# Kernel tuning notes

Hardware: AMD Instinct MI355X
Metric: run time of the kernel (lower is better)

## Reference

```python
import jax, jax.numpy as jnp
import numpy as np

B, T, H, IN, OUT, HORIZON = 65536, 15, 128, 6, 3, 10
LN_EPS = 1e-5


def _w(k, shape, s=0.08):
    return jax.random.normal(k, shape, jnp.float32) * s


def setup_inputs() -> dict:
    key = jax.random.key(0)
    ks = jax.random.split(key, 16)
    return {
        "x": jax.random.normal(ks[0], (B, T, IN), jnp.float32),
        # encoder layer 0 (input 6 -> 128), PyTorch LSTM gate order i,f,g,o
        "W_ih0": _w(ks[1], (4 * H, IN)), "W_hh0": _w(ks[2], (4 * H, H)), "b0": jnp.zeros((4 * H,), jnp.float32),
        # encoder layer 1 (128 -> 128)
        "W_ih1": _w(ks[3], (4 * H, H)), "W_hh1": _w(ks[4], (4 * H, H)), "b1": jnp.zeros((4 * H,), jnp.float32),
        # decoder LSTM (128 -> 128)
        "W_ihd": _w(ks[5], (4 * H, H)), "W_hhd": _w(ks[6], (4 * H, H)), "bd": jnp.zeros((4 * H,), jnp.float32),
        # step embedding [pred_horizon+1, H]
        "emb": _w(ks[7], (HORIZON + 1, H), 0.5),
        # decoder_input_proj: Linear(3+128 -> 128)
        "Wp": _w(ks[8], (H, OUT + H)), "bp": jnp.zeros((H,), jnp.float32),
        # heads
        "Wm": _w(ks[9], (OUT, H)), "bm": jnp.zeros((OUT,), jnp.float32),
        "Ws": _w(ks[10], (OUT, H)), "bs": jnp.zeros((OUT,), jnp.float32),
        # dec_ln
        "ln_g": jnp.ones((H,), jnp.float32), "ln_b": jnp.zeros((H,), jnp.float32),
    }


def _lstm_cell(h, c, x_t, Wih, Whh, b):
    g = x_t @ Wih.T + h @ Whh.T + b  # [B, 4H]
    i, f, gg, o = jnp.split(g, 4, axis=-1)
    c = jax.nn.sigmoid(f) * c + jax.nn.sigmoid(i) * jnp.tanh(gg)
    h = jax.nn.sigmoid(o) * jnp.tanh(c)
    return h, c


def _run_lstm_layer(seq, Wih, Whh, b):
    # seq: [B, T, D] -> outputs [B, T, H], final (h, c)
    n = seq.shape[0]
    h0 = jnp.zeros((n, H), seq.dtype)
    c0 = jnp.zeros((n, H), seq.dtype)

    def step(carry, xt):
        h, c = carry
        h, c = _lstm_cell(h, c, xt, Wih, Whh, b)
        return (h, c), h

    (h, c), outs = jax.lax.scan(step, (h0, c0), jnp.swapaxes(seq, 0, 1))
    return jnp.swapaxes(outs, 0, 1), h, c


def _layernorm(x, g, b):
    mu = jnp.mean(x, axis=-1, keepdims=True)
    var = jnp.mean(jnp.square(x - mu), axis=-1, keepdims=True)
    return (x - mu) * jax.lax.rsqrt(var + LN_EPS) * g + b


def reference(x, W_ih0, W_hh0, b0, W_ih1, W_hh1, b1, W_ihd, W_hhd, bd, emb, Wp, bp, Wm, bm, Ws, bs, ln_g, ln_b):
    # --- encoder: 2-layer LSTM (eval mode, no dropout) ---
    out0, _, _ = _run_lstm_layer(x, W_ih0, W_hh0, b0)
    _, h_enc, c_enc = _run_lstm_layer(out0, W_ih1, W_hh1, b1)

    prev0 = x[:, -1, :OUT]  # [B, 3]
    n = x.shape[0]

    def dstep(carry, step):
        h, c, prev = carry
        se = jnp.broadcast_to(emb[step], (n, H))
        dec_in = jax.nn.relu(jnp.concatenate([prev, se], axis=-1) @ Wp.T + bp)
        h, c = _lstm_cell(h, c, dec_in, W_ihd, W_hhd, bd)
        feat = _layernorm(h, ln_g, ln_b)
        mu = feat @ Wm.T + bm
        ls = jnp.clip(feat @ Ws.T + bs, -6.0, 3.0)
        prev = jax.lax.stop_gradient(mu)  # mu.detach()
        return (h, c, prev), (mu, ls)

    _, (mus, lss) = jax.lax.scan(dstep, (h_enc, c_enc, prev0), jnp.arange(HORIZON))
    means = jnp.swapaxes(mus, 0, 1)     # [B, HORIZON, 3]
    log_stds = jnp.swapaxes(lss, 0, 1)  # [B, HORIZON, 3]
    return means, log_stds
```

## Files before the change

### kernel.cpp

```cpp
#include <hip/hip_runtime.h>
#include <stdint.h>

typedef __attribute__((ext_vector_type(8))) short short8;
typedef __attribute__((ext_vector_type(4))) float f32x4;

#define NT 15

#define SET0 0
#define SET1 81920
#define SET2 212992
#define SET3 344064
#define PK_TOTAL 346112
#define DD_OFF (PK_TOTAL*2)

__device__ __forceinline__ unsigned short f2bf(float f){
  unsigned int u = __builtin_bit_cast(unsigned int, f);
  u += 0x7fffu + ((u >> 16) & 1u);
  return (unsigned short)(u >> 16);
}
__device__ __forceinline__ float sigf(float x){
  return __builtin_amdgcn_rcpf(1.0f + __expf(-x));
}
__device__ __forceinline__ float tanhf_(float x){
  return 1.0f - 2.0f*__builtin_amdgcn_rcpf(1.0f + __expf(2.0f*x));
}
__device__ __forceinline__ int sidx(int row, int col){
  return row*128 + (col ^ ((row & 7) << 3));
}
__device__ __forceinline__ void BAR(){
  asm volatile("s_waitcnt lgkmcnt(0)" ::: "memory");
  __builtin_amdgcn_s_barrier();
}

__global__ void pack_w(const float* __restrict__ Wih0, const float* __restrict__ Whh0,
                       const float* __restrict__ Wih1, const float* __restrict__ Whh1,
                       const float* __restrict__ Wihd, const float* __restrict__ Whhd,
                       const float* __restrict__ Wm,  const float* __restrict__ Ws,
                       unsigned short* __restrict__ pk)
{
  int idx = blockIdx.x*256 + threadIdx.x;
  if (idx >= PK_TOTAL) return;
  float v = 0.f;
  if (idx >= SET3){
    int e = idx - SET3;
    int j = e & 7, lane = (e >> 3) & 63, kt = e >> 9;
    int n = lane & 15;
    int k = kt*32 + (lane >> 4)*8 + j;
    if (n < 3) v = Wm[n*128 + k];
    else if (n < 6) v = Ws[(n-3)*128 + k];
  } else {
    int set, e;
    if (idx < SET1){ set = 0; e = idx; }
    else if (idx < SET2){ set = 1; e = idx - SET1; }
    else { set = 2; e = idx - SET2; }
    int j = e & 7, lane = (e >> 3) & 63, rest = e >> 9;
    int nf = (set == 0) ? 5 : 8;
    int kt = rest % nf, pair = rest / nf;
    int g = pair & 3, jt = pair >> 2;
    int n = g*128 + jt*16 + (lane & 15);
    int kk = (lane >> 4)*8 + j;
    if (set == 0){
      if (kt < 4) v = Whh0[n*128 + kt*32 + kk];
      else if (kk < 6) v = Wih0[n*6 + kk];
    } else {
      const float* Wi = (set == 1) ? Wih1 : Wihd;
      const float* Wh = (set == 1) ? Whh1 : Whhd;
      v = (kt < 4) ? Wi[n*128 + kt*32 + kk] : Wh[n*128 + (kt-4)*32 + kk];
    }
  }
  pk[idx] = f2bf(v);
}

__global__ void prep_dec(const float* __restrict__ emb, const float* __restrict__ Wp,
                         const float* __restrict__ bp,
                         const float* __restrict__ Wm, const float* __restrict__ Ws,
                         const float* __restrict__ bm, const float* __restrict__ bs,
                         const float* __restrict__ lng, const float* __restrict__ lnb,
                         float* __restrict__ dd)
{
  int idx = blockIdx.x*128 + threadIdx.x;
  if (idx < 1280){
    int s = idx >> 7, j = idx & 127;
    float acc = bp[j];
    for (int k = 0; k < 128; ++k) acc += emb[s*128 + k] * Wp[j*131 + 3 + k];
    dd[idx] = acc;
  } else if (idx < 2048){
    int e = idx - 1280; int o = e >> 7, j = e & 127;
    const float* W = (o < 3) ? (Wm + o*128) : (Ws + (o-3)*128);
    dd[idx] = W[j] * lng[j];
  } else if (idx < 2054){
    int o = idx - 2048;
    const float* W = (o < 3) ? (Wm + o*128) : (Ws + (o-3)*128);
    float a = 0.f;
    for (int k = 0; k < 128; ++k) a += W[k]*lng[k];
    dd[idx] = a;
  } else if (idx < 2060){
    int o = idx - 2054;
    const float* W = (o < 3) ? (Wm + o*128) : (Ws + (o-3)*128);
    float a = (o < 3) ? bm[o] : bs[o-3];
    for (int k = 0; k < 128; ++k) a += W[k]*lnb[k];
    dd[idx] = a;
  }
}

__global__ __launch_bounds__(512, 2)
void traj_main(const float* __restrict__ x,
               const unsigned short* __restrict__ pk,
               const float* __restrict__ dd,
               const float* __restrict__ b0g, const float* __restrict__ b1g,
               const float* __restrict__ bdg,
               const float* __restrict__ Wp,
               float* __restrict__ out)
{
  __shared__ __align__(16) unsigned short hP[3][64*128];
  __shared__ __align__(16) union {
    unsigned short xs[NT*64*8];
    struct { float om[64][30]; float os[64][30]; } o;
  } u2;
  __shared__ __align__(16) struct {
    float sred[8][64][8];
    float prevb[64][4];
  } u;

  const int tid  = threadIdx.x;
  const int w    = tid >> 6;
  const int lane = tid & 63;
  const int lidx = lane & 15;
  const int lgrp = lane >> 4;
  const int col  = w*16 + lidx;
  const int row0 = blockIdx.x * 64;

  for (int i = tid; i < 64*128; i += 512){ hP[0][i] = 0; hP[1][i] = 0; }
  for (int i = tid; i < NT*64*8; i += 512){
    int k8 = i & 7, rt = i >> 3;
    int r = rt & 63, t = rt >> 6;
    u2.xs[i] = (k8 < 6) ? f2bf(x[(size_t)(row0 + r)*90 + t*6 + k8])
                        : (unsigned short)0;
  }

  float b0v[4], b1v[4];
  #pragma unroll
  for (int g = 0; g < 4; ++g){ b0v[g] = b0g[g*128 + col]; b1v[g] = b1g[g*128 + col]; }

  float c0[4][4], c1[4][4];
  #pragma unroll
  for (int m = 0; m < 4; ++m)
    #pragma unroll
    for (int r = 0; r < 4; ++r){ c0[m][r] = 0.f; c1[m][r] = 0.f; }

  __syncthreads();

  const unsigned short* pw0 = pk + SET0 + (w*4)*(5*512) + lane*8;
  const unsigned short* pw1 = pk + SET1 + (w*4)*(8*512) + lane*8;
  const unsigned short* pw2 = pk + SET2 + (w*4)*(8*512) + lane*8;
  const short8 z8 = {0,0,0,0,0,0,0,0};

  int i0 = 0, i1 = 1, ifr = 2;
  #pragma unroll 1
  for (int t = 0; t < NT; ++t){
    const unsigned short* bh0 = &hP[i0][0];
    const unsigned short* bh1 = &hP[i1][0];
    unsigned short*       bnw = &hP[ifr][0];

    {
      f32x4 acc[4][4];
      #pragma unroll
      for (int m = 0; m < 4; ++m)
        #pragma unroll
        for (int g = 0; g < 4; ++g)
          acc[m][g] = (f32x4){b0v[g], b0v[g], b0v[g], b0v[g]};
      #pragma unroll
      for (int kt = 0; kt < 5; ++kt){
        short8 am[4];
        #pragma unroll
        for (int m = 0; m < 4; ++m){
          if (kt < 4)
            am[m] = *(const short8*)&bh0[sidx(m*16 + lidx, kt*32 + lgrp*8)];
          else
            am[m] = (lgrp == 0) ? *(const short8*)&u2.xs[(t*64 + m*16 + lidx)*8] : z8;
        }
        #pragma unroll
        for (int g = 0; g < 4; ++g){
          short8 wv = *(const short8*)&pw0[(g*5 + kt)*512];
          #pragma unroll
          for (int m = 0; m < 4; ++m)
            acc[m][g] = __builtin_amdgcn_mfma_f32_16x16x32_bf16(am[m], wv, acc[m][g], 0, 0, 0);
        }
      }
      #pragma unroll
      for (int m = 0; m < 4; ++m)
        #pragma unroll
        for (int r = 0; r < 4; ++r){
          float iv = sigf(acc[m][0][r]);
          float fv = sigf(acc[m][1][r]);
          float gv = tanhf_(acc[m][2][r]);
          float ov = sigf(acc[m][3][r]);
          float c = fv*c0[m][r] + iv*gv;
          c0[m][r] = c;
          bnw[sidx(m*16 + lgrp*4 + r, col)] = f2bf(ov*tanhf_(c));
        }
    }
    BAR();

    {
      f32x4 acc[4][4];
      #pragma unroll
      for (int m = 0; m < 4; ++m)
        #pragma unroll
        for (int g = 0; g < 4; ++g)
          acc[m][g] = (f32x4){b1v[g], b1v[g], b1v[g], b1v[g]};
      #pragma unroll
      for (int kt = 0; kt < 8; ++kt){
        short8 am[4];
        #pragma unroll
        for (int m = 0; m < 4; ++m){
          if (kt < 4)
            am[m] = *(const short8*)&bnw[sidx(m*16 + lidx, kt*32 + lgrp*8)];
          else
            am[m] = *(const short8*)&bh1[sidx(m*16 + lidx, (kt-4)*32 + lgrp*8)];
        }
        #pragma unroll
        for (int g = 0; g < 4; ++g){
          short8 wv = *(const short8*)&pw1[(g*8 + kt)*512];
          #pragma unroll
          for (int m = 0; m < 4; ++m)
            acc[m][g] = __builtin_amdgcn_mfma_f32_16x16x32_bf16(am[m], wv, acc[m][g], 0, 0, 0);
        }
      }
      unsigned short* bwr = const_cast<unsigned short*>(bh0);
      #pragma unroll
      for (int m = 0; m < 4; ++m)
        #pragma unroll
        for (int r = 0; r < 4; ++r){
          float iv = sigf(acc[m][0][r]);
          float fv = sigf(acc[m][1][r]);
          float gv = tanhf_(acc[m][2][r]);
          float ov = sigf(acc[m][3][r]);
          float c = fv*c1[m][r] + iv*gv;
          c1[m][r] = c;
          bwr[sidx(m*16 + lgrp*4 + r, col)] = f2bf(ov*tanhf_(c));
        }
    }
    BAR();
    int t0 = i0; i0 = ifr; ifr = i1; i1 = t0;
  }

  const float* dbase = dd;
  const float* hwp   = dd + 1280;
  const float* hbp   = dd + 2048;
  const float* hcp   = dd + 2054;

  const float wpa = Wp[col*131 + 0], wpb = Wp[col*131 + 1], wpc = Wp[col*131 + 2];
  float bdv[4];
  #pragma unroll
  for (int g = 0; g < 4; ++g) bdv[g] = bdg[g*128 + col];
  float hwv[6], hbv[6], hcv[6];
  #pragma unroll
  for (int o = 0; o < 6; ++o){
    hwv[o] = hwp[o*128 + col];
    hbv[o] = hbp[o];
    hcv[o] = hcp[o];
  }

  if (tid < 192){
    int r = tid / 3, o = tid - r*3;
    u.prevb[r][o] = x[(size_t)(row0 + r)*90 + 14*6 + o];
  }
  __syncthreads();

  int hcur = 1, hnew = 0;
  #pragma unroll 1
  for (int s = 0; s < 10; ++s){
    unsigned short* bdin = &hP[2][0];
    const unsigned short* bh = &hP[hcur][0];
    unsigned short* bhn = &hP[hnew][0];

    const float dbs = dbase[s*128 + col];
    #pragma unroll
    for (int m = 0; m < 4; ++m)
      #pragma unroll
      for (int r = 0; r < 4; ++r){
        const int row = m*16 + lgrp*4 + r;
        f32x4 pv = *(const f32x4*)&u.prevb[row][0];
        float v = dbs + pv[0]*wpa + pv[1]*wpb + pv[2]*wpc;
        bdin[sidx(row, col)] = f2bf(v > 0.f ? v : 0.f);
      }
    BAR();

    {
      f32x4 acc[4][4];
      #pragma unroll
      for (int m = 0; m < 4; ++m)
        #pragma unroll
        for (int g = 0; g < 4; ++g)
          acc[m][g] = (f32x4){bdv[g], bdv[g], bdv[g], bdv[g]};
      #pragma unroll
      for (int kt = 0; kt < 8; ++kt){
        short8 am[4];
        #pragma unroll
        for (int m = 0; m < 4; ++m){
          if (kt < 4)
            am[m] = *(const short8*)&bdin[sidx(m*16 + lidx, kt*32 + lgrp*8)];
          else
            am[m] = *(const short8*)&bh[sidx(m*16 + lidx, (kt-4)*32 + lgrp*8)];
        }
        #pragma unroll
        for (int g = 0; g < 4; ++g){
          short8 wv = *(const short8*)&pw2[(g*8 + kt)*512];
          #pragma unroll
          for (int m = 0; m < 4; ++m)
            acc[m][g] = __builtin_amdgcn_mfma_f32_16x16x32_bf16(am[m], wv, acc[m][g], 0, 0, 0);
        }
      }
      #pragma unroll
      for (int m = 0; m < 4; ++m)
        #pragma unroll
        for (int r = 0; r < 4; ++r){
          float iv = sigf(acc[m][0][r]);
          float fv = sigf(acc[m][1][r]);
          float gv = tanhf_(acc[m][2][r]);
          float ov = sigf(acc[m][3][r]);
          float c = fv*c1[m][r] + iv*gv;
          c1[m][r] = c;
          float h = ov*tanhf_(c);
          const int row = m*16 + lgrp*4 + r;
          bhn[sidx(row, col)] = f2bf(h);
          float vals[8];
          vals[0] = h; vals[1] = h*h;
          #pragma unroll
          for (int o = 0; o < 6; ++o) vals[2+o] = h*hwv[o];
          #pragma unroll
          for (int d = 1; d < 16; d <<= 1)
            #pragma unroll
            for (int k = 0; k < 8; ++k)
              vals[k] += __shfl_xor(vals[k], d);
          if (lidx == 0){
            *(f32x4*)&u.sred[w][row][0] = (f32x4){vals[0], vals[1], vals[2], vals[3]};
            *(f32x4*)&u.sred[w][row][4] = (f32x4){vals[4], vals[5], vals[6], vals[7]};
          }
        }
    }
    BAR();

    if (tid < 64){
      float s1 = 0.f, s2 = 0.f;
      float A[6] = {0.f, 0.f, 0.f, 0.f, 0.f, 0.f};
      #pragma unroll
      for (int ww = 0; ww < 8; ++ww){
        f32x4 v0 = *(const f32x4*)&u.sred[ww][tid][0];
        f32x4 v1 = *(const f32x4*)&u.sred[ww][tid][4];
        s1 += v0[0]; s2 += v0[1];
        A[0] += v0[2]; A[1] += v0[3];
        A[2] += v1[0]; A[3] += v1[1]; A[4] += v1[2]; A[5] += v1[3];
      }
      float mu = s1 * (1.f/128.f);
      float var = s2 * (1.f/128.f) - mu*mu;
      float rs = __builtin_amdgcn_rsqf(var + 1e-5f);
      #pragma unroll
      for (int o = 0; o < 3; ++o){
        float v = rs*(A[o] - mu*hbv[o]) + hcv[o];
        u2.o.om[tid][s*3 + o] = v;
        u.prevb[tid][o] = v;
      }
      #pragma unroll
      for (int o = 3; o < 6; ++o){
        float v = rs*(A[o] - mu*hbv[o]) + hcv[o];
        u2.o.os[tid][s*3 + (o-3)] = fminf(fmaxf(v, -6.f), 3.f);
      }
    }
    BAR();
    int tswap = hcur; hcur = hnew; hnew = tswap;
  }

  for (int i = tid; i < 1920; i += 512){
    int r = i / 30, cx = i - r*30;
    out[(size_t)(row0 + r)*30 + cx] = u2.o.om[r][cx];
    out[(size_t)65536*30 + (size_t)(row0 + r)*30 + cx] = u2.o.os[r][cx];
  }
}

extern "C" void kernel_launch(void* const* d_in, const int* in_sizes, int n_in,
                              void* d_out, int out_size, void* d_ws, size_t ws_size,
                              hipStream_t stream)
{
  const float* x    = (const float*)d_in[0];
  const float* Wih0 = (const float*)d_in[1];
  const float* Whh0 = (const float*)d_in[2];
  const float* b0   = (const float*)d_in[3];
  const float* Wih1 = (const float*)d_in[4];
  const float* Whh1 = (const float*)d_in[5];
  const float* b1   = (const float*)d_in[6];
  const float* Wihd = (const float*)d_in[7];
  const float* Whhd = (const float*)d_in[8];
  const float* bd   = (const float*)d_in[9];
  const float* emb  = (const float*)d_in[10];
  const float* Wp   = (const float*)d_in[11];
  const float* bp   = (const float*)d_in[12];
  const float* Wm   = (const float*)d_in[13];
  const float* bm   = (const float*)d_in[14];
  const float* Ws   = (const float*)d_in[15];
  const float* bs   = (const float*)d_in[16];
  const float* lng  = (const float*)d_in[17];
  const float* lnb  = (const float*)d_in[18];

  unsigned short* pkw = (unsigned short*)d_ws;
  float* dd = (float*)((char*)d_ws + DD_OFF);

  pack_w<<<(PK_TOTAL + 255)/256, 256, 0, stream>>>(Wih0, Whh0, Wih1, Whh1,
                                                   Wihd, Whhd, Wm, Ws, pkw);
  prep_dec<<<17, 128, 0, stream>>>(emb, Wp, bp, Wm, Ws, bm, bs, lng, lnb, dd);
  traj_main<<<1024, 512, 0, stream>>>(x, pkw, dd, b0, b1, bd, Wp, (float*)d_out);
}
```

Measured before the change: 2.074 ms.

## Wavefront-skew encoder layers to halve barriers per timestep

Restructures the two-layer encoder loop so layer 0 at step k and layer 1 at step k-1 run in the same iteration, reading double-buffered hidden states, with one barrier per iteration instead of two. Shared memory grows from three to four hidden-state buffers, which may affect occupancy at two blocks per CU. The loop runs one extra iteration for the pipeline prologue and epilogue, and buffer indices in the decoder are remapped to match.

```diff
diff --git a/kernel.cpp b/kernel.cpp
--- a/kernel.cpp
+++ b/kernel.cpp
@@ -112,7 +112,8 @@
                const float* __restrict__ Wp,
                float* __restrict__ out)
 {
-  __shared__ __align__(16) unsigned short hP[3][64*128];
+  __shared__ __align__(16) unsigned short hA[2][64*128];
+  __shared__ __align__(16) unsigned short hB[2][64*128];
   __shared__ __align__(16) union {
     unsigned short xs[NT*64*8];
     struct { float om[64][30]; float os[64][30]; } o;
@@ -130,7 +131,7 @@
   const int col  = w*16 + lidx;
   const int row0 = blockIdx.x * 64;
 
-  for (int i = tid; i < 64*128; i += 512){ hP[0][i] = 0; hP[1][i] = 0; }
+  for (int i = tid; i < 64*128; i += 512){ hA[1][i] = 0; hB[1][i] = 0; }
   for (int i = tid; i < NT*64*8; i += 512){
     int k8 = i & 7, rt = i >> 3;
     int r = rt & 63, t = rt >> 6;
@@ -155,14 +156,14 @@
   const unsigned short* pw2 = pk + SET2 + (w*4)*(8*512) + lane*8;
   const short8 z8 = {0,0,0,0,0,0,0,0};
 
-  int i0 = 0, i1 = 1, ifr = 2;
   #pragma unroll 1
-  for (int t = 0; t < NT; ++t){
-    const unsigned short* bh0 = &hP[i0][0];
-    const unsigned short* bh1 = &hP[i1][0];
-    unsigned short*       bnw = &hP[ifr][0];
-
-    {
+  for (int k = 0; k <= NT; ++k){
+    const unsigned short* h0rd = &hA[(k+1)&1][0];
+    unsigned short*       h0wr = &hA[k&1][0];
+    const unsigned short* h1rd = &hB[k&1][0];
+    unsigned short*       h1wr = &hB[(k+1)&1][0];
+
+    if (k < NT){
       f32x4 acc[4][4];
       #pragma unroll
       for (int m = 0; m < 4; ++m)
@@ -174,10 +175,11 @@
         short8 am[4];
         #pragma unroll
         for (int m = 0; m < 4; ++m){
+          const int arow = m*16 + lidx;
           if (kt < 4)
-            am[m] = *(const short8*)&bh0[sidx(m*16 + lidx, kt*32 + lgrp*8)];
+            am[m] = *(const short8*)&h0rd[sidx(arow, kt*32 + lgrp*8)];
           else
-            am[m] = (lgrp == 0) ? *(const short8*)&u2.xs[(t*64 + m*16 + lidx)*8] : z8;
+            am[m] = (lgrp == 0) ? *(const short8*)&u2.xs[(k*64 + arow)*8] : z8;
         }
         #pragma unroll
         for (int g = 0; g < 4; ++g){
@@ -197,12 +199,11 @@
           float ov = sigf(acc[m][3][r]);
           float c = fv*c0[m][r] + iv*gv;
           c0[m][r] = c;
-          bnw[sidx(m*16 + lgrp*4 + r, col)] = f2bf(ov*tanhf_(c));
+          h0wr[sidx(m*16 + lgrp*4 + r, col)] = f2bf(ov*tanhf_(c));
         }
     }
-    BAR();
-
-    {
+
+    if (k >= 1){
       f32x4 acc[4][4];
       #pragma unroll
       for (int m = 0; m < 4; ++m)
@@ -214,10 +215,11 @@
         short8 am[4];
         #pragma unroll
         for (int m = 0; m < 4; ++m){
+          const int arow = m*16 + lidx;
           if (kt < 4)
-            am[m] = *(const short8*)&bnw[sidx(m*16 + lidx, kt*32 + lgrp*8)];
+            am[m] = *(const short8*)&h0rd[sidx(arow, kt*32 + lgrp*8)];
           else
-            am[m] = *(const short8*)&bh1[sidx(m*16 + lidx, (kt-4)*32 + lgrp*8)];
+            am[m] = *(const short8*)&h1rd[sidx(arow, (kt-4)*32 + lgrp*8)];
         }
         #pragma unroll
         for (int g = 0; g < 4; ++g){
@@ -227,7 +229,6 @@
             acc[m][g] = __builtin_amdgcn_mfma_f32_16x16x32_bf16(am[m], wv, acc[m][g], 0, 0, 0);
         }
       }
-      unsigned short* bwr = const_cast<unsigned short*>(bh0);
       #pragma unroll
       for (int m = 0; m < 4; ++m)
         #pragma unroll
@@ -238,11 +239,10 @@
           float ov = sigf(acc[m][3][r]);
           float c = fv*c1[m][r] + iv*gv;
           c1[m][r] = c;
-          bwr[sidx(m*16 + lgrp*4 + r, col)] = f2bf(ov*tanhf_(c));
+          h1wr[sidx(m*16 + lgrp*4 + r, col)] = f2bf(ov*tanhf_(c));
         }
     }
     BAR();
-    int t0 = i0; i0 = ifr; ifr = i1; i1 = t0;
   }
 
   const float* dbase = dd;
@@ -268,12 +268,12 @@
   }
   __syncthreads();
 
-  int hcur = 1, hnew = 0;
+  int hcur = 0, hnew = 1;
   #pragma unroll 1
   for (int s = 0; s < 10; ++s){
-    unsigned short* bdin = &hP[2][0];
-    const unsigned short* bh = &hP[hcur][0];
-    unsigned short* bhn = &hP[hnew][0];
+    unsigned short* bdin = &hA[0][0];
+    const unsigned short* bh = &hB[hcur][0];
+    unsigned short* bhn = &hB[hnew][0];
 
     const float dbs = dbase[s*128 + col];
     #pragma unroll
@@ -299,10 +299,11 @@
         short8 am[4];
         #pragma unroll
         for (int m = 0; m < 4; ++m){
+          const int arow = m*16 + lidx;
           if (kt < 4)
-            am[m] = *(const short8*)&bdin[sidx(m*16 + lidx, kt*32 + lgrp*8)];
+            am[m] = *(const short8*)&bdin[sidx(arow, kt*32 + lgrp*8)];
           else
-            am[m] = *(const short8*)&bh[sidx(m*16 + lidx, (kt-4)*32 + lgrp*8)];
+            am[m] = *(const short8*)&bh[sidx(arow, (kt-4)*32 + lgrp*8)];
         }
         #pragma unroll
         for (int g = 0; g < 4; ++g){
@@ -332,8 +333,8 @@
           #pragma unroll
           for (int d = 1; d < 16; d <<= 1)
             #pragma unroll
-            for (int k = 0; k < 8; ++k)
-              vals[k] += __shfl_xor(vals[k], d);
+            for (int kk = 0; kk < 8; ++kk)
+              vals[kk] += __shfl_xor(vals[kk], d);
           if (lidx == 0){
             *(f32x4*)&u.sred[w][row][0] = (f32x4){vals[0], vals[1], vals[2], vals[3]};
             *(f32x4*)&u.sred[w][row][4] = (f32x4){vals[4], vals[5], vals[6], vals[7]};
```

Measured after the change: 2.038 ms. No clear change (-1.8%).
